# Kernel tuning notes

Measured on AMD Instinct MI355X. Metric: run time of the kernel, lower is better.

## Reference

```python
import jax, jax.numpy as jnp
import numpy as np

N, L, D = 32, 1568, 768
HEADS = 12
PART = 49
SCALE = (D // HEADS) ** (-0.5)


def setup_inputs() -> dict:
    key = jax.random.key(0)
    k1, k2, k3, k4, k5 = jax.random.split(key, 5)
    x = jax.random.normal(k1, (N, L, D), dtype=jnp.float32)
    w_qkv = jax.random.normal(k2, (3 * D, D), dtype=jnp.float32) * 0.02
    w_proj = jax.random.normal(k3, (D, D), dtype=jnp.float32) * 0.02
    b_proj = jax.random.normal(k4, (D,), dtype=jnp.float32) * 0.02
    # per-sample random permutation = argsort of uniform noise (as in source)
    noise = jax.random.uniform(k5, (N, L))
    shuffle_ids = jnp.argsort(noise, axis=-1).astype(jnp.int64)
    return {"x": x, "w_qkv": w_qkv, "w_proj": w_proj, "b_proj": b_proj,
            "shuffle_ids": shuffle_ids}


def reference(x, w_qkv, w_proj, b_proj, shuffle_ids):
    # qkv projection (no bias: qkv_bias=False)
    qkv = jnp.einsum('nld,ed->nle', x, w_qkv)          # [N, L, 3D]
    q, k, v = jnp.split(qkv, 3, axis=-1)               # each [N, L, D]
    # gather k, v by random permutation (q_shuffle=False: q not gathered)
    idx = shuffle_ids[..., None]                        # [N, L, 1]
    k = jnp.take_along_axis(k, idx, axis=1)
    v = jnp.take_along_axis(v, idx, axis=1)
    dh = D // HEADS
    # FAITHFUL to source bug: q is overwritten by k (`q = k.view(...)`)
    q = k.reshape(-1, PART, HEADS, dh)                  # [N*L/P, P, H, dh]
    kk = k.reshape(-1, PART, HEADS, dh)
    vv = v.reshape(-1, PART, HEADS, dh)
    attn = jnp.einsum('nqhd,nkhd->nqkh', q, kk) * SCALE  # [P', P, P, H]
    attn = jax.nn.softmax(attn, axis=-2)                 # softmax over k axis
    out = jnp.einsum('nqkh,nkhd->nqhd', attn, vv)        # [P', P, H, dh]
    out = out.reshape(N, L, D)  # note: left in shuffled order (q_shuffle=False)
    out = jnp.einsum('nld,ed->nle', out, w_proj) + b_proj
    return out
```

## Files before the change

### kernel.cpp

```cpp
#include <hip/hip_runtime.h>

typedef unsigned short u16;
typedef unsigned int u32;
typedef float f32x4 __attribute__((ext_vector_type(4)));
typedef __bf16 bf16x8 __attribute__((ext_vector_type(8)));

__device__ __forceinline__ u16 f2bf(float f) {
  u32 b = __float_as_uint(f);
  b += 0x7fffu + ((b >> 16) & 1u);
  return (u16)(b >> 16);
}

__device__ __forceinline__ void gload16(const void* g, void* l) {
  __builtin_amdgcn_global_load_lds(
      (const __attribute__((address_space(1))) void*)g,
      (__attribute__((address_space(3))) void*)l, 16, 0, 0);
}

__global__ __launch_bounds__(256)
void cvt_f32_bf16(const float4* __restrict__ in, ushort4* __restrict__ out, int n4) {
  int i = blockIdx.x * blockDim.x + threadIdx.x;
  int stride = gridDim.x * blockDim.x;
  for (; i < n4; i += stride) {
    float4 v = in[i];
    ushort4 o;
    o.x = f2bf(v.x); o.y = f2bf(v.y); o.z = f2bf(v.z); o.w = f2bf(v.w);
    out[i] = o;
  }
}

template<bool BF16OUT>
__global__ __launch_bounds__(256)
void gemm_bt(const u16* __restrict__ A, const u16* __restrict__ B,
             u16* __restrict__ Cb, float* __restrict__ Cf,
             const float* __restrict__ bias, int N, int K)
{
  __shared__ u16 As[128 * 32];
  __shared__ u16 Bs[128 * 32];
  const int tid = threadIdx.x;
  const int lane = tid & 63;
  const int wid = tid >> 6;
  const int wr = (wid >> 1) * 64;
  const int wc = (wid & 1) * 64;
  const int row0 = blockIdx.y * 128;
  const int col0 = blockIdx.x * 128;
  const int rlo = lane & 15, g4 = lane >> 4;

  f32x4 acc[4][4] = {};

  const int u0 = wid * 64 + lane;
  const int nk = K >> 5;
  for (int kt = 0; kt < nk; ++kt) {
    __syncthreads();
    #pragma unroll
    for (int i = 0; i < 2; ++i) {
      int u = u0 + i * 256;
      const u16* ga = A + (size_t)(row0 + (u >> 2)) * K + kt * 32 + (u & 3) * 8;
      gload16(ga, &As[(wid * 64 + i * 256) * 8]);
      const u16* gb = B + (size_t)(col0 + (u >> 2)) * K + kt * 32 + (u & 3) * 8;
      gload16(gb, &Bs[(wid * 64 + i * 256) * 8]);
    }
    __syncthreads();
    bf16x8 a[4], b[4];
    #pragma unroll
    for (int m = 0; m < 4; ++m)
      a[m] = *(const bf16x8*)&As[(wr + m * 16 + rlo) * 32 + g4 * 8];
    #pragma unroll
    for (int nn = 0; nn < 4; ++nn)
      b[nn] = *(const bf16x8*)&Bs[(wc + nn * 16 + rlo) * 32 + g4 * 8];
    #pragma unroll
    for (int m = 0; m < 4; ++m)
      #pragma unroll
      for (int nn = 0; nn < 4; ++nn)
        acc[m][nn] = __builtin_amdgcn_mfma_f32_16x16x32_bf16(a[m], b[nn], acc[m][nn], 0, 0, 0);
  }
  #pragma unroll
  for (int m = 0; m < 4; ++m) {
    #pragma unroll
    for (int nn = 0; nn < 4; ++nn) {
      int row = row0 + wr + m * 16 + g4 * 4;
      int col = col0 + wc + nn * 16 + rlo;
      #pragma unroll
      for (int v = 0; v < 4; ++v) {
        if (BF16OUT) {
          Cb[(size_t)(row + v) * N + col] = f2bf(acc[m][nn][v]);
        } else {
          Cf[(size_t)(row + v) * N + col] = acc[m][nn][v] + bias[col];
        }
      }
    }
  }
}

__global__ __launch_bounds__(64)
void attn_part(const u16* __restrict__ kv, const int* __restrict__ ids,
               u16* __restrict__ out)
{
  __shared__ u16 Ksw[64 * 64];
  __shared__ u16 Vt[64 * 64];
  __shared__ int rowg[64];
  const int lane = threadIdx.x;
  const int p = blockIdx.x / 12;
  const int h = blockIdx.x - p * 12;
  const int n = p >> 5;
  const int lbase = (p & 31) * 49;

  if (lane < 49) rowg[lane] = n * 1568 + ids[n * 1568 + lbase + lane];
  __syncthreads();

  const int rr8 = lane >> 3, c16 = lane & 7;
  #pragma unroll
  for (int it = 0; it < 8; ++it) {
    int r = it * 8 + rr8;
    uint4 val = {0, 0, 0, 0};
    if (r < 49) val = *(const uint4*)(kv + (size_t)rowg[r] * 1536 + h * 64 + c16 * 8);
    *(uint4*)&Ksw[r * 64 + ((c16 ^ (r & 7)) * 8)] = val;
  }
  #pragma unroll
  for (int it = 0; it < 8; ++it) {
    int r = it * 8 + rr8;
    uint4 val = {0, 0, 0, 0};
    if (r < 49) val = *(const uint4*)(kv + (size_t)rowg[r] * 1536 + 768 + h * 64 + c16 * 8);
    const u16* vs = (const u16*)&val;
    #pragma unroll
    for (int j = 0; j < 8; ++j) {
      int d = c16 * 8 + j;
      Vt[d * 64 + (((r >> 3) ^ (d & 7)) * 8) + (r & 7)] = vs[j];
    }
  }
  __syncthreads();

  const int rlo = lane & 15, g4 = lane >> 4;
  bf16x8 af[4][2];
  #pragma unroll
  for (int m = 0; m < 4; ++m)
    #pragma unroll
    for (int g = 0; g < 2; ++g) {
      int row = m * 16 + rlo;
      af[m][g] = *(const bf16x8*)&Ksw[row * 64 + (((g * 4 + g4) ^ (row & 7)) * 8)];
    }
  f32x4 s[4][4] = {};
  #pragma unroll
  for (int m = 0; m < 4; ++m)
    #pragma unroll
    for (int nf = 0; nf < 4; ++nf)
      #pragma unroll
      for (int g = 0; g < 2; ++g)
        s[m][nf] = __builtin_amdgcn_mfma_f32_16x16x32_bf16(af[m][g], af[nf][g], s[m][nf], 0, 0, 0);

  #pragma unroll
  for (int m = 0; m < 4; ++m) {
    #pragma unroll
    for (int v = 0; v < 4; ++v) {
      float mx = -1e30f;
      #pragma unroll
      for (int nf = 0; nf < 4; ++nf) {
        float x = s[m][nf][v] * 0.125f;
        int col = nf * 16 + rlo;
        x = (col < 49) ? x : -1e30f;
        s[m][nf][v] = x;
        mx = fmaxf(mx, x);
      }
      #pragma unroll
      for (int d = 1; d < 16; d <<= 1) mx = fmaxf(mx, __shfl_xor(mx, d));
      float sum = 0.f;
      #pragma unroll
      for (int nf = 0; nf < 4; ++nf) {
        int col = nf * 16 + rlo;
        float e = (col < 49) ? __expf(s[m][nf][v] - mx) : 0.f;
        s[m][nf][v] = e;
        sum += e;
      }
      #pragma unroll
      for (int d = 1; d < 16; d <<= 1) sum += __shfl_xor(sum, d);
      float inv = 1.0f / sum;
      #pragma unroll
      for (int nf = 0; nf < 4; ++nf) s[m][nf][v] *= inv;
    }
  }

  __syncthreads();
  #pragma unroll
  for (int m = 0; m < 4; ++m)
    #pragma unroll
    for (int nf = 0; nf < 4; ++nf)
      #pragma unroll
      for (int v = 0; v < 4; ++v) {
        int R = m * 16 + g4 * 4 + v;
        int C = nf * 16 + rlo;
        Ksw[R * 64 + (((C >> 3) ^ (R & 7)) * 8) + (C & 7)] = f2bf(s[m][nf][v]);
      }
  __syncthreads();

  bf16x8 pa[4][2], vb[4][2];
  #pragma unroll
  for (int m = 0; m < 4; ++m)
    #pragma unroll
    for (int g = 0; g < 2; ++g) {
      int row = m * 16 + rlo;
      pa[m][g] = *(const bf16x8*)&Ksw[row * 64 + (((g * 4 + g4) ^ (row & 7)) * 8)];
    }
  #pragma unroll
  for (int nd = 0; nd < 4; ++nd)
    #pragma unroll
    for (int g = 0; g < 2; ++g) {
      int row = nd * 16 + rlo;
      vb[nd][g] = *(const bf16x8*)&Vt[row * 64 + (((g * 4 + g4) ^ (row & 7)) * 8)];
    }
  f32x4 o[4][4] = {};
  #pragma unroll
  for (int m = 0; m < 4; ++m)
    #pragma unroll
    for (int nd = 0; nd < 4; ++nd)
      #pragma unroll
      for (int g = 0; g < 2; ++g)
        o[m][nd] = __builtin_amdgcn_mfma_f32_16x16x32_bf16(pa[m][g], vb[nd][g], o[m][nd], 0, 0, 0);

  #pragma unroll
  for (int m = 0; m < 4; ++m)
    #pragma unroll
    for (int nd = 0; nd < 4; ++nd)
      #pragma unroll
      for (int v = 0; v < 4; ++v) {
        int q = m * 16 + g4 * 4 + v;
        if (q < 49) {
          size_t token = (size_t)p * 49 + q;
          out[token * 768 + h * 64 + nd * 16 + rlo] = f2bf(o[m][nd][v]);
        }
      }
}

extern "C" void kernel_launch(void* const* d_in, const int* in_sizes, int n_in,
                              void* d_out, int out_size, void* d_ws, size_t ws_size,
                              hipStream_t stream) {
  const float* x      = (const float*)d_in[0];
  const float* w_qkv  = (const float*)d_in[1];
  const float* w_proj = (const float*)d_in[2];
  const float* b_proj = (const float*)d_in[3];
  const int*   ids    = (const int*)d_in[4];
  float* outp = (float*)d_out;

  char* ws = (char*)d_ws;
  u16* kvbuf = (u16*)ws;
  u16* xbuf  = (u16*)(ws + 154140672);
  u16* wkv   = (u16*)(ws + 154140672 + 77070336);
  u16* wproj = (u16*)(ws + 154140672 + 77070336 + 2359296);

  auto cgrid = [](int n4) { int g = (n4 + 255) / 256; return g > 2048 ? 2048 : g; };

  cvt_f32_bf16<<<cgrid(9633792), 256, 0, stream>>>((const float4*)x, (ushort4*)xbuf, 9633792);
  cvt_f32_bf16<<<cgrid(294912), 256, 0, stream>>>((const float4*)(w_qkv + 768 * 768), (ushort4*)wkv, 294912);
  cvt_f32_bf16<<<cgrid(147456), 256, 0, stream>>>((const float4*)w_proj, (ushort4*)wproj, 147456);

  dim3 g1(12, 392);
  gemm_bt<true><<<g1, 256, 0, stream>>>(xbuf, wkv, kvbuf, nullptr, nullptr, 1536, 768);

  attn_part<<<12288, 64, 0, stream>>>(kvbuf, ids, xbuf);

  dim3 g2(6, 392);
  gemm_bt<false><<<g2, 256, 0, stream>>>(xbuf, wproj, nullptr, outp, b_proj, 768, 768);
}
```

Measured before the change: 632.0 us.

## Replace GEMM with 256x256 tile, 8-wave, double-buffered pipelined kernel with XCD swizzle

Both projection GEMMs now use a new kernel with 256x256 output tiles, 512 threads, and BK=64. Global-to-LDS loads are staged in quarter-tiles across a double buffer and interleaved with MFMA phases under raw barriers, explicit waitcnt and setprio. LDS uses an XOR swizzle to avoid bank conflicts, and workgroup IDs are remapped so neighbouring tiles land on the same XCD for L2 reuse. The aim is to hide memory latency and raise MFMA utilisation. The cost is much higher register and LDS pressure, plus fragile manual synchronisation that depends on exact vmcnt accounting.

```diff
diff --git a/kernel.cpp b/kernel.cpp
--- a/kernel.cpp
+++ b/kernel.cpp
@@ -15,6 +15,12 @@
   __builtin_amdgcn_global_load_lds(
       (const __attribute__((address_space(1))) void*)g,
       (__attribute__((address_space(3))) void*)l, 16, 0, 0);
+}
+
+__device__ __forceinline__ int xcd_swz(int wgid, int nwg) {
+  const int q = nwg >> 3, r = nwg & 7;
+  const int xcd = wgid & 7, pos = wgid >> 3;
+  return (xcd < r ? xcd * (q + 1) : r * (q + 1) + (xcd - r) * q) + pos;
 }
 
 __global__ __launch_bounds__(256)
@@ -30,62 +36,141 @@
 }
 
 template<bool BF16OUT>
-__global__ __launch_bounds__(256)
-void gemm_bt(const u16* __restrict__ A, const u16* __restrict__ B,
+__global__ __launch_bounds__(512, 2)
+void gemm256(const u16* __restrict__ A, const u16* __restrict__ B,
              u16* __restrict__ Cb, float* __restrict__ Cf,
-             const float* __restrict__ bias, int N, int K)
+             const float* __restrict__ bias, int N, int K, int gx)
 {
-  __shared__ u16 As[128 * 32];
-  __shared__ u16 Bs[128 * 32];
+  __shared__ u16 LDS[2][4][8192];
   const int tid = threadIdx.x;
   const int lane = tid & 63;
   const int wid = tid >> 6;
-  const int wr = (wid >> 1) * 64;
-  const int wc = (wid & 1) * 64;
-  const int row0 = blockIdx.y * 128;
-  const int col0 = blockIdx.x * 128;
+  const int wm = wid >> 2, wn = wid & 3;
   const int rlo = lane & 15, g4 = lane >> 4;
 
-  f32x4 acc[4][4] = {};
-
-  const int u0 = wid * 64 + lane;
-  const int nk = K >> 5;
-  for (int kt = 0; kt < nk; ++kt) {
-    __syncthreads();
+  const int id = xcd_swz(blockIdx.x, gridDim.x);
+  const int by = id / gx, bx = id - by * gx;
+  const int row0 = by * 256, col0 = bx * 256;
+  const int nk = K >> 6;
+
+  const int sr = tid >> 3;
+  const int c_phys = (tid & 7) * 16;
+
+  auto stage = [&](int h) {
+    int kt = h >> 2; if (kt > nk - 1) kt = nk - 1;
+    const int type = h & 3;
+    const u16* src = (type < 2) ? B : A;
+    const int rbase = ((type < 2) ? col0 : row0) + (type & 1) * 128;
+    const int slot = (type < 2) ? (2 + (type & 1)) : (type - 2);
+    const int buf = (h >> 2) & 1;
     #pragma unroll
     for (int i = 0; i < 2; ++i) {
-      int u = u0 + i * 256;
-      const u16* ga = A + (size_t)(row0 + (u >> 2)) * K + kt * 32 + (u & 3) * 8;
-      gload16(ga, &As[(wid * 64 + i * 256) * 8]);
-      const u16* gb = B + (size_t)(col0 + (u >> 2)) * K + kt * 32 + (u & 3) * 8;
-      gload16(gb, &Bs[(wid * 64 + i * 256) * 8]);
-    }
-    __syncthreads();
-    bf16x8 a[4], b[4];
-    #pragma unroll
-    for (int m = 0; m < 4; ++m)
-      a[m] = *(const bf16x8*)&As[(wr + m * 16 + rlo) * 32 + g4 * 8];
-    #pragma unroll
-    for (int nn = 0; nn < 4; ++nn)
-      b[nn] = *(const bf16x8*)&Bs[(wc + nn * 16 + rlo) * 32 + g4 * 8];
-    #pragma unroll
-    for (int m = 0; m < 4; ++m)
-      #pragma unroll
-      for (int nn = 0; nn < 4; ++nn)
-        acc[m][nn] = __builtin_amdgcn_mfma_f32_16x16x32_bf16(a[m], b[nn], acc[m][nn], 0, 0, 0);
-  }
-  #pragma unroll
-  for (int m = 0; m < 4; ++m) {
-    #pragma unroll
-    for (int nn = 0; nn < 4; ++nn) {
-      int row = row0 + wr + m * 16 + g4 * 4;
-      int col = col0 + wc + nn * 16 + rlo;
+      int r = sr + i * 64;
+      int c_log = c_phys ^ (((r >> 1) & 7) << 4);
+      const u16* g = src + (size_t)(rbase + r) * K + kt * 64 + (c_log >> 1);
+      gload16(g, &LDS[buf][slot][wid * 512 + i * 4096]);
+    }
+  };
+  auto ldA = [&](int buf, int m8, int ks) -> bf16x8 {
+    int row = wm * 128 + m8 * 16 + rlo;
+    int r = row & 127;
+    int col = (ks * 32 + g4 * 8) ^ (((r >> 1) & 7) << 3);
+    return *(const bf16x8*)&LDS[buf][row >> 7][r * 64 + col];
+  };
+  auto ldB = [&](int buf, int n, int ks) -> bf16x8 {
+    int row = wn * 64 + n * 16 + rlo;
+    int r = row & 127;
+    int col = (ks * 32 + g4 * 8) ^ (((r >> 1) & 7) << 3);
+    return *(const bf16x8*)&LDS[buf][2 + (row >> 7)][r * 64 + col];
+  };
+
+  f32x4 acc[8][4] = {};
+  bf16x8 bf[4][2], af[4][2];
+
+  #pragma unroll
+  for (int h = 0; h < 7; ++h) stage(h);
+  asm volatile("s_waitcnt vmcnt(6)" ::: "memory");
+  __builtin_amdgcn_s_barrier();
+
+  for (int t = 0; t < nk; ++t) {
+    const int buf = t & 1;
+    #pragma unroll
+    for (int n = 0; n < 4; ++n)
+      #pragma unroll
+      for (int ks = 0; ks < 2; ++ks) bf[n][ks] = ldB(buf, n, ks);
+    #pragma unroll
+    for (int m = 0; m < 4; ++m)
+      #pragma unroll
+      for (int ks = 0; ks < 2; ++ks) af[m][ks] = ldA(buf, m, ks);
+    stage(4 * t + 7);
+    __builtin_amdgcn_s_barrier();
+    asm volatile("s_waitcnt lgkmcnt(0)" ::: "memory");
+    __builtin_amdgcn_s_setprio(1);
+    #pragma unroll
+    for (int m = 0; m < 4; ++m)
+      #pragma unroll
+      for (int ks = 0; ks < 2; ++ks) {
+        acc[m][0] = __builtin_amdgcn_mfma_f32_16x16x32_bf16(af[m][ks], bf[0][ks], acc[m][0], 0, 0, 0);
+        acc[m][1] = __builtin_amdgcn_mfma_f32_16x16x32_bf16(af[m][ks], bf[1][ks], acc[m][1], 0, 0, 0);
+      }
+    __builtin_amdgcn_s_setprio(0);
+    __builtin_amdgcn_s_barrier();
+    stage(4 * t + 8);
+    __builtin_amdgcn_s_barrier();
+    __builtin_amdgcn_s_setprio(1);
+    #pragma unroll
+    for (int m = 0; m < 4; ++m)
+      #pragma unroll
+      for (int ks = 0; ks < 2; ++ks) {
+        acc[m][2] = __builtin_amdgcn_mfma_f32_16x16x32_bf16(af[m][ks], bf[2][ks], acc[m][2], 0, 0, 0);
+        acc[m][3] = __builtin_amdgcn_mfma_f32_16x16x32_bf16(af[m][ks], bf[3][ks], acc[m][3], 0, 0, 0);
+      }
+    __builtin_amdgcn_s_setprio(0);
+    __builtin_amdgcn_s_barrier();
+    #pragma unroll
+    for (int m = 0; m < 4; ++m)
+      #pragma unroll
+      for (int ks = 0; ks < 2; ++ks) af[m][ks] = ldA(buf, 4 + m, ks);
+    stage(4 * t + 9);
+    __builtin_amdgcn_s_barrier();
+    asm volatile("s_waitcnt lgkmcnt(0)" ::: "memory");
+    __builtin_amdgcn_s_setprio(1);
+    #pragma unroll
+    for (int m = 0; m < 4; ++m)
+      #pragma unroll
+      for (int ks = 0; ks < 2; ++ks) {
+        acc[4 + m][0] = __builtin_amdgcn_mfma_f32_16x16x32_bf16(af[m][ks], bf[0][ks], acc[4 + m][0], 0, 0, 0);
+        acc[4 + m][1] = __builtin_amdgcn_mfma_f32_16x16x32_bf16(af[m][ks], bf[1][ks], acc[4 + m][1], 0, 0, 0);
+      }
+    __builtin_amdgcn_s_setprio(0);
+    __builtin_amdgcn_s_barrier();
+    stage(4 * t + 10);
+    __builtin_amdgcn_s_barrier();
+    __builtin_amdgcn_s_setprio(1);
+    #pragma unroll
+    for (int m = 0; m < 4; ++m)
+      #pragma unroll
+      for (int ks = 0; ks < 2; ++ks) {
+        acc[4 + m][2] = __builtin_amdgcn_mfma_f32_16x16x32_bf16(af[m][ks], bf[2][ks], acc[4 + m][2], 0, 0, 0);
+        acc[4 + m][3] = __builtin_amdgcn_mfma_f32_16x16x32_bf16(af[m][ks], bf[3][ks], acc[4 + m][3], 0, 0, 0);
+      }
+    __builtin_amdgcn_s_setprio(0);
+    asm volatile("s_waitcnt vmcnt(6)" ::: "memory");
+    __builtin_amdgcn_s_barrier();
+  }
+
+  #pragma unroll
+  for (int m = 0; m < 8; ++m) {
+    #pragma unroll
+    for (int n = 0; n < 4; ++n) {
+      int row = row0 + wm * 128 + m * 16 + g4 * 4;
+      int col = col0 + wn * 64 + n * 16 + rlo;
       #pragma unroll
       for (int v = 0; v < 4; ++v) {
         if (BF16OUT) {
-          Cb[(size_t)(row + v) * N + col] = f2bf(acc[m][nn][v]);
+          Cb[(size_t)(row + v) * N + col] = f2bf(acc[m][n][v]);
         } else {
-          Cf[(size_t)(row + v) * N + col] = acc[m][nn][v] + bias[col];
+          Cf[(size_t)(row + v) * N + col] = acc[m][n][v] + bias[col];
         }
       }
     }
@@ -252,11 +337,9 @@
   cvt_f32_bf16<<<cgrid(294912), 256, 0, stream>>>((const float4*)(w_qkv + 768 * 768), (ushort4*)wkv, 294912);
   cvt_f32_bf16<<<cgrid(147456), 256, 0, stream>>>((const float4*)w_proj, (ushort4*)wproj, 147456);
 
-  dim3 g1(12, 392);
-  gemm_bt<true><<<g1, 256, 0, stream>>>(xbuf, wkv, kvbuf, nullptr, nullptr, 1536, 768);
+  gemm256<true><<<dim3(6 * 196), 512, 0, stream>>>(xbuf, wkv, kvbuf, nullptr, nullptr, 1536, 768, 6);
 
   attn_part<<<12288, 64, 0, stream>>>(kvbuf, ids, xbuf);
 
-  dim3 g2(6, 392);
-  gemm_bt<false><<<g2, 256, 0, stream>>>(xbuf, wproj, nullptr, outp, b_proj, 768, 768);
-}
+  gemm256<false><<<dim3(3 * 196), 512, 0, stream>>>(xbuf, wproj, nullptr, outp, b_proj, 768, 768, 3);
+}
```

Result: faster. 574.4 us (-9.1%).
